# Optimization experiments

Measured on AMD Instinct MI355X. Metric: run time of the kernel, lower is better.

## Reference

```python
import jax, jax.numpy as jnp
import numpy as np

B, C, HW, SCALE = 8, 512, 64, 8
M = C // SCALE  # Q/K channel dim
EPS = 1e-6


def setup_inputs() -> dict:
    key = jax.random.key(0)
    ks = jax.random.split(key, 8)
    s = 0.02
    return {
        "x": jax.random.normal(ks[0], (B, C, HW, HW), dtype=jnp.float32),
        "wq": jax.random.normal(ks[1], (M, C), dtype=jnp.float32) * s,
        "bq": jax.random.normal(ks[2], (M,), dtype=jnp.float32) * s,
        "wk": jax.random.normal(ks[3], (M, C), dtype=jnp.float32) * s,
        "bk": jax.random.normal(ks[4], (M,), dtype=jnp.float32) * s,
        "wv": jax.random.normal(ks[5], (C, C), dtype=jnp.float32) * s,
        "bv": jax.random.normal(ks[6], (C,), dtype=jnp.float32) * s,
        "gamma": jax.random.normal(ks[7], (1,), dtype=jnp.float32),
    }


def reference(x, wq, bq, wk, bk, wv, bv, gamma):
    b, c, w, h = x.shape
    n = w * h
    xf = x.reshape(b, c, n)  # [B,C,N]
    # 1x1 convs == channel GEMMs
    Q = jnp.einsum('bcn,mc->bmn', xf, wq) + bq[None, :, None]  # [B,M,N]
    K = jnp.einsum('bcn,mc->bmn', xf, wk) + bk[None, :, None]  # [B,M,N]
    V = jnp.einsum('bcn,oc->bon', xf, wv) + bv[None, :, None]  # [B,C,N]
    # pooling gate: global max + global avg over spatial dims -> [B,C,1]
    gate = (jnp.max(xf, axis=-1) + jnp.mean(xf, axis=-1))[:, :, None]
    V = gate * V
    Qf = jax.nn.softplus(Q).transpose(0, 2, 1)  # [B,N,M]
    Kf = jax.nn.softplus(K)                      # [B,M,N]
    KV = jnp.einsum('bmn,bcn->bmc', Kf, V)       # [B,M,C]
    norm = 1.0 / jnp.einsum('bnm,bm->bn', Qf, jnp.sum(Kf, axis=-1) + EPS)  # [B,N]
    wval = jnp.einsum('bnm,bmc,bn->bcn', Qf, KV, norm)  # [B,C,N]
    wval = wval.reshape(b, c, h, w)
    return x + gamma * wval
```

## Files before the change

### kernel.cpp

```cpp
#include <hip/hip_runtime.h>
#include <math.h>

#define Bb 8
#define Cc 512
#define Nn 4096
#define Mm 64
#define OC 640
#define EPSf 1e-6f

typedef unsigned short ushort_t;
typedef unsigned int uint_t;
typedef __attribute__((ext_vector_type(8))) short short8;
typedef __attribute__((ext_vector_type(4))) float f32x4;

constexpr size_t OFF_GATE = 0;
constexpr size_t OFF_BCAT = OFF_GATE + (size_t)Bb * Cc;
constexpr size_t OFF_GPM  = OFF_BCAT + (size_t)OC;
constexpr size_t OFF_GPS  = OFF_GPM + (size_t)64 * Bb * Cc;
constexpr size_t OFF_WBF  = OFF_GPS + (size_t)64 * Bb * Cc;
constexpr size_t OFF_XT   = OFF_WBF + (size_t)OC * Cc / 2;
constexpr size_t OFF_QBF  = OFF_XT + (size_t)Bb * Nn * Cc / 2;
constexpr size_t OFF_KBF  = OFF_QBF + (size_t)Bb * Mm * Nn / 2;
constexpr size_t OFF_VBF  = OFF_KBF + (size_t)Bb * Mm * Nn / 2;
constexpr size_t OFF_KVBF = OFF_VBF + (size_t)Bb * Cc * Nn / 2;
constexpr size_t OFF_KSUM = OFF_KVBF + (size_t)Bb * Cc * Mm / 2;
constexpr size_t OFF_NORM = OFF_KSUM + (size_t)Bb * Mm;
constexpr size_t OFF_QT   = OFF_NORM + (size_t)Bb * Nn;

__device__ __forceinline__ float softplus_f(float v) {
    return fmaxf(v, 0.f) + __logf(1.f + __expf(-fabsf(v)));
}
__device__ __forceinline__ ushort_t f2bf(float f) {
    uint_t u = __float_as_uint(f);
    uint_t r = (u + 0x7fffu + ((u >> 16) & 1u)) >> 16;
    return (ushort_t)r;
}
__device__ __forceinline__ float bf2f(ushort_t h) {
    return __uint_as_float(((uint_t)h) << 16);
}
__device__ __forceinline__ void gload_lds16(const void* g, void* l) {
    __builtin_amdgcn_global_load_lds(
        (const __attribute__((address_space(1))) unsigned int*)g,
        (__attribute__((address_space(3))) unsigned int*)l, 16, 0, 0);
}
#define BARRIER()   asm volatile("s_barrier" ::: "memory")
#define WAIT_VM(N)  asm volatile("s_waitcnt vmcnt(" #N ")" ::: "memory")

__global__ void wconv_k(const float* __restrict__ wq, const float* __restrict__ bq,
                        const float* __restrict__ wk, const float* __restrict__ bk,
                        const float* __restrict__ wv, const float* __restrict__ bv,
                        ushort_t* __restrict__ wbf, float* __restrict__ bcat) {
    int i = blockIdx.x * 256 + threadIdx.x;
    if (i < OC * Cc) {
        int o = i / Cc, c = i % Cc;
        float v;
        if (o < Mm)            v = wq[o * Cc + c];
        else if (o < 2 * Mm)   v = wk[(o - Mm) * Cc + c];
        else                   v = wv[(o - 2 * Mm) * Cc + c];
        wbf[i] = f2bf(v);
    }
    if (i < OC) {
        float v;
        if (i < Mm)            v = bq[i];
        else if (i < 2 * Mm)   v = bk[i - Mm];
        else                   v = bv[i - 2 * Mm];
        bcat[i] = v;
    }
}

__global__ __launch_bounds__(256) void xtrans_k(const float* __restrict__ x, ushort_t* __restrict__ xT,
                                                float* __restrict__ gpm, float* __restrict__ gps) {
    const int nb = blockIdx.x * 64;
    const int cb = blockIdx.y * 64;
    const int b  = blockIdx.z;
    __shared__ float Xt[64][65];
    __shared__ float pmx[4][64], psm[4][64];
    const int t = threadIdx.x;
    #pragma unroll
    for (int r = 0; r < 16; r++) {
        int cl = (t >> 6) + r * 4;
        int nl = t & 63;
        Xt[cl][nl] = x[((size_t)b * Cc + cb + cl) * Nn + nb + nl];
    }
    __syncthreads();
    #pragma unroll
    for (int r = 0; r < 8; r++) {
        int nl = (t >> 5) + r * 8;
        int c0 = (t & 31) * 2;
        uint_t pk = (uint_t)f2bf(Xt[c0][nl]) | ((uint_t)f2bf(Xt[c0 + 1][nl]) << 16);
        *(uint_t*)(xT + ((size_t)b * Nn + nb + nl) * Cc + cb + c0) = pk;
    }
    {
        int cl = t & 63, q = t >> 6;
        float mx = -3.4e38f, sm = 0.f;
        #pragma unroll
        for (int j = 0; j < 16; j++) {
            float v = Xt[cl][q * 16 + j];
            mx = fmaxf(mx, v); sm += v;
        }
        pmx[q][cl] = mx; psm[q][cl] = sm;
    }
    __syncthreads();
    if (t < 64) {
        float mx = fmaxf(fmaxf(pmx[0][t], pmx[1][t]), fmaxf(pmx[2][t], pmx[3][t]));
        float sm = psm[0][t] + psm[1][t] + psm[2][t] + psm[3][t];
        size_t idx = (size_t)blockIdx.x * (Bb * Cc) + (size_t)b * Cc + cb + t;
        gpm[idx] = mx;
        gps[idx] = sm;
    }
}

__global__ void gatered_k(const float* __restrict__ gpm, const float* __restrict__ gps,
                          float* __restrict__ gate) {
    int bc = blockIdx.x;
    int l = threadIdx.x;
    float mx = gpm[(size_t)l * (Bb * Cc) + bc];
    float sm = gps[(size_t)l * (Bb * Cc) + bc];
    #pragma unroll
    for (int off = 32; off; off >>= 1) {
        mx = fmaxf(mx, __shfl_xor(mx, off));
        sm += __shfl_xor(sm, off);
    }
    if (l == 0) gate[bc] = mx + sm * (1.f / Nn);
}

__global__ __launch_bounds__(64) void qkv_mfma_k(const ushort_t* __restrict__ wbf,
                                                 const ushort_t* __restrict__ xT,
                                                 const float* __restrict__ bcat,
                                                 ushort_t* __restrict__ Qbf,
                                                 ushort_t* __restrict__ Kbf,
                                                 ushort_t* __restrict__ Vbf) {
    const int nb = blockIdx.x * 64;
    const int ot = blockIdx.y;
    const int b  = blockIdx.z;
    __shared__ ushort_t At[2][2048];
    __shared__ ushort_t Bt[2][2048];
    const int lane = threadIdx.x;
    const int hi = lane >> 4, lo = lane & 15;
    const int rwl = lane >> 2;
    const int kc  = (((lane & 3) ^ ((lane >> 3) & 3)) * 8);
    const int sx  = (hi ^ ((lo >> 1) & 3)) * 8;
    const ushort_t* xb = xT + (size_t)b * Nn * Cc;
    const ushort_t* wb = wbf + (size_t)ot * 64 * Cc;

    f32x4 acc[4][4] = {};

    auto stage = [&](int buf, int kb) {
        #pragma unroll
        for (int li = 0; li < 4; li++) {
            const int rw = li * 16 + rwl;
            gload_lds16(wb + (size_t)rw * Cc + kb + kc, &At[buf][li * 512]);
        }
        #pragma unroll
        for (int li = 0; li < 4; li++) {
            const int rw = li * 16 + rwl;
            gload_lds16(xb + (size_t)(nb + rw) * Cc + kb + kc, &Bt[buf][li * 512]);
        }
    };
    auto compute = [&](int buf) {
        short8 a[4], bfr[4];
        #pragma unroll
        for (int mi = 0; mi < 4; mi++)
            a[mi] = *(const short8*)(&At[buf][(mi * 16 + lo) * 32 + sx]);
        #pragma unroll
        for (int ni = 0; ni < 4; ni++)
            bfr[ni] = *(const short8*)(&Bt[buf][(ni * 16 + lo) * 32 + sx]);
        #pragma unroll
        for (int mi = 0; mi < 4; mi++)
            #pragma unroll
            for (int ni = 0; ni < 4; ni++)
                acc[mi][ni] = __builtin_amdgcn_mfma_f32_16x16x32_bf16(a[mi], bfr[ni], acc[mi][ni], 0, 0, 0);
    };

    stage(0, 0);
    #pragma unroll
    for (int t = 0; t < 16; ++t) {
        __builtin_amdgcn_sched_barrier(0);
        if (t < 15) {
            stage((t + 1) & 1, (t + 1) * 32);
            WAIT_VM(8);
        } else {
            WAIT_VM(0);
        }
        compute(t & 1);
    }

    ushort_t* dst0;
    if (ot == 0)      dst0 = Qbf + (size_t)b * Mm * Nn;
    else if (ot == 1) dst0 = Kbf + (size_t)b * Mm * Nn;
    else              dst0 = Vbf + ((size_t)b * Cc + (ot - 2) * 64) * Nn;

    if (ot < 2) {
        #pragma unroll
        for (int mi = 0; mi < 4; mi++)
            #pragma unroll
            for (int r = 0; r < 4; r++) {
                const int ol = mi * 16 + hi * 4 + r;
                const float bias = bcat[ot * 64 + ol];
                ushort_t* dst = dst0 + (size_t)ol * Nn + nb;
                #pragma unroll
                for (int ni = 0; ni < 4; ni++)
                    dst[ni * 16 + lo] = f2bf(softplus_f(acc[mi][ni][r] + bias));
            }
    } else {
        #pragma unroll
        for (int mi = 0; mi < 4; mi++)
            #pragma unroll
            for (int r = 0; r < 4; r++) {
                const int ol = mi * 16 + hi * 4 + r;
                const float bias = bcat[ot * 64 + ol];
                ushort_t* dst = dst0 + (size_t)ol * Nn + nb;
                #pragma unroll
                for (int ni = 0; ni < 4; ni++)
                    dst[ni * 16 + lo] = f2bf(acc[mi][ni][r] + bias);
            }
    }
}

__global__ __launch_bounds__(256) void ksum_k(const ushort_t* __restrict__ Kbf, float* __restrict__ Ksum) {
    int bm = blockIdx.x;
    const ushort_t* row = Kbf + (size_t)bm * Nn;
    int t = threadIdx.x;
    float sm = 0.f;
    for (int i = t * 8; i < Nn; i += 2048) {
        short8 v = *(const short8*)(row + i);
        #pragma unroll
        for (int j = 0; j < 8; j++) sm += bf2f((ushort_t)v[j]);
    }
    #pragma unroll
    for (int off = 32; off; off >>= 1) sm += __shfl_xor(sm, off);
    __shared__ float ssm[4];
    if ((t & 63) == 0) ssm[t >> 6] = sm;
    __syncthreads();
    if (t == 0) Ksum[bm] = ssm[0] + ssm[1] + ssm[2] + ssm[3];
}

__global__ __launch_bounds__(256, 3) void kv_mfma_k(const ushort_t* __restrict__ Kbf,
                                                    const ushort_t* __restrict__ Vbf,
                                                    float* __restrict__ KVpart) {
    const int cb = blockIdx.x * 128;
    const int split = blockIdx.y;
    const int b = blockIdx.z;
    __shared__ ushort_t Vt[2][4096];
    __shared__ ushort_t Kt[2][2048];
    const int tid = threadIdx.x;
    const int w = tid >> 6, lane = tid & 63;
    const int hi = lane >> 4, lo = lane & 15;
    const int rwl = lane >> 2;
    const int kc  = (((lane & 3) ^ ((lane >> 3) & 3)) * 8);
    const int sx  = (hi ^ ((lo >> 1) & 3)) * 8;
    const ushort_t* Vb = Vbf + (size_t)b * Cc * Nn;
    const ushort_t* Kb = Kbf + (size_t)b * Mm * Nn;
    const int nbase = split * 512;

    f32x4 acc[2][4] = {};

    auto stage = [&](int buf, int n0) {
        #pragma unroll
        for (int li = 0; li < 2; li++) {
            const int rw = (w * 2 + li) * 16 + rwl;
            gload_lds16(Vb + (size_t)(cb + rw) * Nn + n0 + kc, &Vt[buf][(w * 2 + li) * 512]);
        }
        gload_lds16(Kb + (size_t)(w * 16 + rwl) * Nn + n0 + kc, &Kt[buf][w * 512]);
    };
    auto compute = [&](int buf) {
        short8 a[2], bv[4];
        #pragma unroll
        for (int mi = 0; mi < 2; mi++)
            a[mi] = *(const short8*)(&Vt[buf][(w * 32 + mi * 16 + lo) * 32 + sx]);
        #pragma unroll
        for (int ni = 0; ni < 4; ni++)
            bv[ni] = *(const short8*)(&Kt[buf][(ni * 16 + lo) * 32 + sx]);
        #pragma unroll
        for (int mi = 0; mi < 2; mi++)
            #pragma unroll
            for (int ni = 0; ni < 4; ni++)
                acc[mi][ni] = __builtin_amdgcn_mfma_f32_16x16x32_bf16(a[mi], bv[ni], acc[mi][ni], 0, 0, 0);
    };

    stage(0, nbase);
    #pragma unroll
    for (int t = 0; t < 16; ++t) {
        if (t < 15) {
            stage((t + 1) & 1, nbase + (t + 1) * 32);
            WAIT_VM(3);
        } else {
            WAIT_VM(0);
        }
        BARRIER();
        compute(t & 1);
        BARRIER();
    }

    float* dst = KVpart + (size_t)(split * Bb + b) * Cc * Mm;
    #pragma unroll
    for (int mi = 0; mi < 2; mi++)
        #pragma unroll
        for (int r = 0; r < 4; r++) {
            const int c = cb + w * 32 + mi * 16 + hi * 4 + r;
            #pragma unroll
            for (int ni = 0; ni < 4; ni++)
                dst[(size_t)c * Mm + ni * 16 + lo] = acc[mi][ni][r];
        }
}

__global__ __launch_bounds__(256) void kvred_k(const float* __restrict__ KVpart,
                                               const float* __restrict__ gate,
                                               ushort_t* __restrict__ KVbf) {
    int i = blockIdx.x * 256 + threadIdx.x;
    const f32x4* p = (const f32x4*)KVpart;
    f32x4 s = p[i];
    #pragma unroll
    for (int sp = 1; sp < 8; sp++) s += p[(size_t)sp * 65536 + i];
    int idx4 = i * 4;
    int b = idx4 >> 15;
    int c = (idx4 >> 6) & (Cc - 1);
    float g = gate[b * Cc + c];
    uint2 pk;
    pk.x = (uint_t)f2bf(s[0] * g) | ((uint_t)f2bf(s[1] * g) << 16);
    pk.y = (uint_t)f2bf(s[2] * g) | ((uint_t)f2bf(s[3] * g) << 16);
    *(uint2*)(KVbf + (size_t)i * 4) = pk;
}

__global__ __launch_bounds__(256) void qtransnorm_k(const ushort_t* __restrict__ Qbf,
                                                    const float* __restrict__ Ksum,
                                                    ushort_t* __restrict__ QT,
                                                    float* __restrict__ normb) {
    const int n0 = blockIdx.x * 64;
    const int b  = blockIdx.y;
    __shared__ float Qs[64][65];
    __shared__ float ks[64];
    __shared__ float ps[4][64];
    const int t = threadIdx.x;
    if (t < 64) ks[t] = Ksum[b * Mm + t] + EPSf;
    {
        int m = t >> 2, q = t & 3;
        const ushort_t* src = Qbf + ((size_t)b * Mm + m) * Nn + n0 + q * 16;
        short8 v0 = *(const short8*)(src);
        short8 v1 = *(const short8*)(src + 8);
        #pragma unroll
        for (int j = 0; j < 8; j++) {
            Qs[m][q * 16 + j]     = bf2f((ushort_t)v0[j]);
            Qs[m][q * 16 + 8 + j] = bf2f((ushort_t)v1[j]);
        }
    }
    __syncthreads();
    {
        int n = t & 63, ch = t >> 6;
        float s = 0.f;
        #pragma unroll
        for (int j = 0; j < 16; j++) s += Qs[ch * 16 + j][n] * ks[ch * 16 + j];
        ps[ch][n] = s;
    }
    __syncthreads();
    if (t < 64) normb[(size_t)b * Nn + n0 + t] = 1.f / (ps[0][t] + ps[1][t] + ps[2][t] + ps[3][t]);
    #pragma unroll
    for (int i = 0; i < 2; i++) {
        int u = t + i * 256;
        int n = u >> 3, j = u & 7;
        short8 v;
        #pragma unroll
        for (int jj = 0; jj < 8; jj++) v[jj] = (short)f2bf(Qs[j * 8 + jj][n]);
        *(short8*)(QT + ((size_t)b * Nn + n0 + n) * Mm + j * 8) = v;
    }
}

__global__ __launch_bounds__(256, 2) void final_mfma_k(const float* __restrict__ x,
                                                       const ushort_t* __restrict__ QT,
                                                       const ushort_t* __restrict__ KVbf,
                                                       const float* __restrict__ normb,
                                                       const float* __restrict__ gamma,
                                                       float* __restrict__ out) {
    const int nb = blockIdx.x * 128;
    const int cb = blockIdx.y * 128;
    const int b  = blockIdx.z;
    __shared__ ushort_t Qs[128 * 64];
    __shared__ ushort_t Ks[128 * 64];
    const int tid  = threadIdx.x;
    const int w    = tid >> 6;
    const int lane = tid & 63;
    const int wr   = w >> 1, wc = w & 1;
    const int hi   = lane >> 4, lo = lane & 15;
    const int lr   = lane >> 3;
    const int swz  = (((lane & 7) ^ (lr & 7)) * 8);
    const ushort_t* Qb = QT + (size_t)b * Nn * Mm;
    const ushort_t* Kb = KVbf + (size_t)b * Cc * Mm;

    #pragma unroll
    for (int p = 0; p < 4; p++) {
        const int rb = p * 32 + w * 8;
        gload_lds16(Qb + (size_t)(nb + rb + lr) * Mm + swz, &Qs[rb * 64]);
        gload_lds16(Kb + (size_t)(cb + rb + lr) * Mm + swz, &Ks[rb * 64]);
    }
    __syncthreads();

    f32x4 acc[4][4] = {};
    #pragma unroll
    for (int kk = 0; kk < 2; kk++) {
        short8 a[4], bfr[4];
        #pragma unroll
        for (int mi = 0; mi < 4; mi++) {
            const int row = wr * 64 + mi * 16 + lo;
            a[mi] = *(const short8*)(&Qs[row * 64 + (((kk * 4 + hi) ^ (lo & 7)) * 8)]);
        }
        #pragma unroll
        for (int ni = 0; ni < 4; ni++) {
            const int row = wc * 64 + ni * 16 + lo;
            bfr[ni] = *(const short8*)(&Ks[row * 64 + (((kk * 4 + hi) ^ (lo & 7)) * 8)]);
        }
        #pragma unroll
        for (int mi = 0; mi < 4; mi++)
            #pragma unroll
            for (int ni = 0; ni < 4; ni++)
                acc[mi][ni] = __builtin_amdgcn_mfma_f32_16x16x32_bf16(a[mi], bfr[ni], acc[mi][ni], 0, 0, 0);
    }

    const float g = gamma[0];
    #pragma unroll
    for (int mi = 0; mi < 4; mi++) {
        const int n0 = nb + wr * 64 + mi * 16 + hi * 4;
        float4 nrm = *(const float4*)(normb + (size_t)b * Nn + n0);
        #pragma unroll
        for (int ni = 0; ni < 4; ni++) {
            const int c = cb + wc * 64 + ni * 16 + lo;
            size_t idx = ((size_t)b * Cc + c) * Nn + n0;
            float4 xv = *(const float4*)(x + idx);
            float4 o;
            o.x = xv.x + g * nrm.x * acc[mi][ni][0];
            o.y = xv.y + g * nrm.y * acc[mi][ni][1];
            o.z = xv.z + g * nrm.z * acc[mi][ni][2];
            o.w = xv.w + g * nrm.w * acc[mi][ni][3];
            *(float4*)(out + idx) = o;
        }
    }
}

extern "C" void kernel_launch(void* const* d_in, const int* in_sizes, int n_in,
                              void* d_out, int out_size, void* d_ws, size_t ws_size,
                              hipStream_t stream) {
    const float* x     = (const float*)d_in[0];
    const float* wq    = (const float*)d_in[1];
    const float* bq    = (const float*)d_in[2];
    const float* wk    = (const float*)d_in[3];
    const float* bk    = (const float*)d_in[4];
    const float* wv    = (const float*)d_in[5];
    const float* bv    = (const float*)d_in[6];
    const float* gamma = (const float*)d_in[7];
    float* out = (float*)d_out;
    float* ws  = (float*)d_ws;

    float*    gate   = ws + OFF_GATE;
    float*    bcat   = ws + OFF_BCAT;
    float*    gpm    = ws + OFF_GPM;
    float*    gps    = ws + OFF_GPS;
    ushort_t* wbf    = (ushort_t*)(ws + OFF_WBF);
    ushort_t* xT     = (ushort_t*)(ws + OFF_XT);
    float*    KVpart = ws + OFF_XT;
    ushort_t* Qbf    = (ushort_t*)(ws + OFF_QBF);
    ushort_t* Kbf    = (ushort_t*)(ws + OFF_KBF);
    ushort_t* Vbf    = (ushort_t*)(ws + OFF_VBF);
    ushort_t* KVbf   = (ushort_t*)(ws + OFF_KVBF);
    float*    Ksum   = ws + OFF_KSUM;
    float*    normb  = ws + OFF_NORM;
    ushort_t* QT     = (ushort_t*)(ws + OFF_QT);

    wconv_k<<<(OC * Cc + 255) / 256, 256, 0, stream>>>(wq, bq, wk, bk, wv, bv, wbf, bcat);
    xtrans_k<<<dim3(Nn / 64, Cc / 64, Bb), 256, 0, stream>>>(x, xT, gpm, gps);
    gatered_k<<<Bb * Cc, 64, 0, stream>>>(gpm, gps, gate);
    qkv_mfma_k<<<dim3(Nn / 64, OC / 64, Bb), 64, 0, stream>>>(wbf, xT, bcat, Qbf, Kbf, Vbf);
    ksum_k<<<Bb * Mm, 256, 0, stream>>>(Kbf, Ksum);
    kv_mfma_k<<<dim3(Cc / 128, 8, Bb), 256, 0, stream>>>(Kbf, Vbf, KVpart);
    kvred_k<<<(Bb * Cc * Mm / 4) / 256, 256, 0, stream>>>(KVpart, gate, KVbf);
    qtransnorm_k<<<dim3(Nn / 64, Bb), 256, 0, stream>>>(Qbf, Ksum, QT, normb);
    final_mfma_k<<<dim3(Nn / 128, Cc / 128, Bb), 256, 0, stream>>>(x, QT, KVbf, normb, gamma, out);
}
```

Measured before the change: 124.2 us.

## Retile QKV GEMM to 4-wave 64x128 blocks with triple-buffered LDS pipeline

The QKV projection GEMM moves from single-wave 64x64 tiles to 256-thread blocks computing 64x128 tiles, with each wave owning a 32x64 sub-tile, so the weight tile is reused across twice as many spatial columns. The k-loop now uses three LDS buffers with a prefetch distance of two and a block barrier per step, replacing the double-buffered single-wave schedule. This reduces redundant weight loads and block count, at the cost of block-level synchronisation and more LDS per block.

```diff
diff --git a/kernel.cpp b/kernel.cpp
--- a/kernel.cpp
+++ b/kernel.cpp
@@ -124,92 +124,85 @@
     if (l == 0) gate[bc] = mx + sm * (1.f / Nn);
 }
 
-__global__ __launch_bounds__(64) void qkv_mfma_k(const ushort_t* __restrict__ wbf,
-                                                 const ushort_t* __restrict__ xT,
-                                                 const float* __restrict__ bcat,
-                                                 ushort_t* __restrict__ Qbf,
-                                                 ushort_t* __restrict__ Kbf,
-                                                 ushort_t* __restrict__ Vbf) {
-    const int nb = blockIdx.x * 64;
-    const int ot = blockIdx.y;
-    const int b  = blockIdx.z;
-    __shared__ ushort_t At[2][2048];
-    __shared__ ushort_t Bt[2][2048];
-    const int lane = threadIdx.x;
-    const int hi = lane >> 4, lo = lane & 15;
-    const int rwl = lane >> 2;
-    const int kc  = (((lane & 3) ^ ((lane >> 3) & 3)) * 8);
-    const int sx  = (hi ^ ((lo >> 1) & 3)) * 8;
-    const ushort_t* xb = xT + (size_t)b * Nn * Cc;
-    const ushort_t* wb = wbf + (size_t)ot * 64 * Cc;
-
-    f32x4 acc[4][4] = {};
+__global__ __launch_bounds__(256, 4) void qkv_mfma_k(const ushort_t* __restrict__ wbf,
+                                                     const ushort_t* __restrict__ xT,
+                                                     const float* __restrict__ bcat,
+                                                     ushort_t* __restrict__ Qbf,
+                                                     ushort_t* __restrict__ Kbf,
+                                                     ushort_t* __restrict__ Vbf) {
+    const int nb  = blockIdx.x * 128;
+    const int oty = blockIdx.y;
+    const int b   = blockIdx.z;
+    __shared__ ushort_t At[3][2048];
+    __shared__ ushort_t Bt[3][4096];
+    const int tid  = threadIdx.x;
+    const int w    = tid >> 6;
+    const int lane = tid & 63;
+    const int wr   = w >> 1, wc = w & 1;
+    const int hi   = lane >> 4, lo = lane & 15;
+    const int rA   = tid >> 2;
+    const int kc   = (((tid & 3) ^ ((tid >> 3) & 3)) * 8);
+    const int sx   = (hi ^ ((lo >> 1) & 3)) * 8;
+    const ushort_t* xb = xT + ((size_t)b * Nn + nb) * Cc;
+    const ushort_t* wb = wbf + (size_t)oty * 64 * Cc;
+
+    f32x4 acc[2][4] = {};
 
     auto stage = [&](int buf, int kb) {
-        #pragma unroll
-        for (int li = 0; li < 4; li++) {
-            const int rw = li * 16 + rwl;
-            gload_lds16(wb + (size_t)rw * Cc + kb + kc, &At[buf][li * 512]);
-        }
-        #pragma unroll
-        for (int li = 0; li < 4; li++) {
-            const int rw = li * 16 + rwl;
-            gload_lds16(xb + (size_t)(nb + rw) * Cc + kb + kc, &Bt[buf][li * 512]);
-        }
+        gload_lds16(wb + (size_t)rA * Cc + kb + kc,        &At[buf][w * 512]);
+        gload_lds16(xb + (size_t)rA * Cc + kb + kc,        &Bt[buf][w * 512]);
+        gload_lds16(xb + (size_t)(64 + rA) * Cc + kb + kc, &Bt[buf][2048 + w * 512]);
     };
     auto compute = [&](int buf) {
-        short8 a[4], bfr[4];
-        #pragma unroll
-        for (int mi = 0; mi < 4; mi++)
-            a[mi] = *(const short8*)(&At[buf][(mi * 16 + lo) * 32 + sx]);
+        short8 a[2], bfr[4];
+        #pragma unroll
+        for (int mi = 0; mi < 2; mi++)
+            a[mi] = *(const short8*)(&At[buf][(wr * 32 + mi * 16 + lo) * 32 + sx]);
         #pragma unroll
         for (int ni = 0; ni < 4; ni++)
-            bfr[ni] = *(const short8*)(&Bt[buf][(ni * 16 + lo) * 32 + sx]);
-        #pragma unroll
-        for (int mi = 0; mi < 4; mi++)
+            bfr[ni] = *(const short8*)(&Bt[buf][(wc * 64 + ni * 16 + lo) * 32 + sx]);
+        #pragma unroll
+        for (int mi = 0; mi < 2; mi++)
             #pragma unroll
             for (int ni = 0; ni < 4; ni++)
                 acc[mi][ni] = __builtin_amdgcn_mfma_f32_16x16x32_bf16(a[mi], bfr[ni], acc[mi][ni], 0, 0, 0);
     };
 
     stage(0, 0);
+    stage(1, 32);
     #pragma unroll
     for (int t = 0; t < 16; ++t) {
-        __builtin_amdgcn_sched_barrier(0);
-        if (t < 15) {
-            stage((t + 1) & 1, (t + 1) * 32);
-            WAIT_VM(8);
-        } else {
-            WAIT_VM(0);
-        }
-        compute(t & 1);
+        if (t < 15) { WAIT_VM(3); } else { WAIT_VM(0); }
+        BARRIER();
+        if (t + 2 < 16) stage((t + 2) % 3, (t + 2) * 32);
+        compute(t % 3);
     }
 
     ushort_t* dst0;
-    if (ot == 0)      dst0 = Qbf + (size_t)b * Mm * Nn;
-    else if (ot == 1) dst0 = Kbf + (size_t)b * Mm * Nn;
-    else              dst0 = Vbf + ((size_t)b * Cc + (ot - 2) * 64) * Nn;
-
-    if (ot < 2) {
-        #pragma unroll
-        for (int mi = 0; mi < 4; mi++)
+    if (oty == 0)      dst0 = Qbf + (size_t)b * Mm * Nn;
+    else if (oty == 1) dst0 = Kbf + (size_t)b * Mm * Nn;
+    else               dst0 = Vbf + ((size_t)b * Cc + (oty - 2) * 64) * Nn;
+
+    if (oty < 2) {
+        #pragma unroll
+        for (int mi = 0; mi < 2; mi++)
             #pragma unroll
             for (int r = 0; r < 4; r++) {
-                const int ol = mi * 16 + hi * 4 + r;
-                const float bias = bcat[ot * 64 + ol];
-                ushort_t* dst = dst0 + (size_t)ol * Nn + nb;
+                const int ol = wr * 32 + mi * 16 + hi * 4 + r;
+                const float bias = bcat[oty * 64 + ol];
+                ushort_t* dst = dst0 + (size_t)ol * Nn + nb + wc * 64;
                 #pragma unroll
                 for (int ni = 0; ni < 4; ni++)
                     dst[ni * 16 + lo] = f2bf(softplus_f(acc[mi][ni][r] + bias));
             }
     } else {
         #pragma unroll
-        for (int mi = 0; mi < 4; mi++)
+        for (int mi = 0; mi < 2; mi++)
             #pragma unroll
             for (int r = 0; r < 4; r++) {
-                const int ol = mi * 16 + hi * 4 + r;
-                const float bias = bcat[ot * 64 + ol];
-                ushort_t* dst = dst0 + (size_t)ol * Nn + nb;
+                const int ol = wr * 32 + mi * 16 + hi * 4 + r;
+                const float bias = bcat[oty * 64 + ol];
+                ushort_t* dst = dst0 + (size_t)ol * Nn + nb + wc * 64;
                 #pragma unroll
                 for (int ni = 0; ni < 4; ni++)
                     dst[ni * 16 + lo] = f2bf(acc[mi][ni][r] + bias);
@@ -467,7 +460,7 @@
     wconv_k<<<(OC * Cc + 255) / 256, 256, 0, stream>>>(wq, bq, wk, bk, wv, bv, wbf, bcat);
     xtrans_k<<<dim3(Nn / 64, Cc / 64, Bb), 256, 0, stream>>>(x, xT, gpm, gps);
     gatered_k<<<Bb * Cc, 64, 0, stream>>>(gpm, gps, gate);
-    qkv_mfma_k<<<dim3(Nn / 64, OC / 64, Bb), 64, 0, stream>>>(wbf, xT, bcat, Qbf, Kbf, Vbf);
+    qkv_mfma_k<<<dim3(Nn / 128, OC / 64, Bb), 256, 0, stream>>>(wbf, xT, bcat, Qbf, Kbf, Vbf);
     ksum_k<<<Bb * Mm, 256, 0, stream>>>(Kbf, Ksum);
     kv_mfma_k<<<dim3(Cc / 128, 8, Bb), 256, 0, stream>>>(Kbf, Vbf, KVpart);
     kvred_k<<<(Bb * Cc * Mm / 4) / 256, 256, 0, stream>>>(KVpart, gate, KVbf);
```

Result: faster. 116.2 us (-6.5%).
